# Kernel tuning notes

Hardware: AMD Instinct MI355X
Metric: run time of the kernel (lower is better)

The kernel has to match this reference:

```python
import jax, jax.numpy as jnp
import numpy as np

NUM_Y_STEPS = 10
NUM_TYPES = 3
ANCHOR_DIM = 3 * NUM_Y_STEPS + 1  # 31
EPS = 1e-9


def setup_inputs() -> dict:
    key = jax.random.key(0)
    k1, k2, k3, k4, k5, k6 = jax.random.split(key, 6)
    B, A = 8192, 26
    D = NUM_TYPES * ANCHOR_DIM  # 93
    pred = jax.random.uniform(k1, (B, A, D), dtype=jnp.float32)
    gt = jax.random.uniform(k2, (B, A, D), dtype=jnp.float32)
    pred_hcam = jax.random.uniform(k3, (B,), dtype=jnp.float32) + 1.0
    gt_hcam = jax.random.uniform(k4, (B,), dtype=jnp.float32) + 1.0
    pred_pitch = jax.random.normal(k5, (B,), dtype=jnp.float32)
    gt_pitch = jax.random.normal(k6, (B,), dtype=jnp.float32)
    return {
        'pred_3D_lanes': pred,
        'gt_3D_lanes': gt,
        'pred_hcam': pred_hcam,
        'gt_hcam': gt_hcam,
        'pred_pitch': pred_pitch,
        'gt_pitch': gt_pitch,
    }


def reference(pred_3D_lanes, gt_3D_lanes, pred_hcam, gt_hcam, pred_pitch, gt_pitch):
    B, A, _ = pred_3D_lanes.shape
    K = NUM_Y_STEPS
    pred = pred_3D_lanes.reshape(B, A, NUM_TYPES, ANCHOR_DIM)
    gt = gt_3D_lanes.reshape(B, A, NUM_TYPES, ANCHOR_DIM)

    pred_class = pred[..., -1:]                # [B,A,T,1]
    pred_anchors = pred[..., : 2 * K]          # [B,A,T,2K]
    pred_vis = pred[..., 2 * K : 3 * K]        # [B,A,T,K]
    gt_class = gt[..., -1:]
    gt_anchors = gt[..., : 2 * K]
    gt_vis = gt[..., 2 * K : 3 * K]

    # loss0: binary cross entropy on visibility (note: (1-gt+eps) as in original)
    loss0 = -jnp.sum(
        gt_vis * jnp.log(pred_vis + EPS)
        + (1.0 - gt_vis + EPS) * jnp.log(1.0 - pred_vis + EPS)
    ) / K

    # loss1: binary cross entropy on lane class probability
    loss1 = -jnp.sum(
        gt_class * jnp.log(pred_class + EPS)
        + (1.0 - gt_class) * jnp.log(1.0 - pred_class + EPS)
    )

    # loss2: visibility/class-masked L1 on X-offset and Z anchors
    vis2 = jnp.concatenate([gt_vis, gt_vis], axis=3)  # [B,A,T,2K]
    loss2 = jnp.sum(jnp.abs(gt_class * vis2 * (pred_anchors - gt_anchors)))

    total = loss0 + loss1 + loss2
    return (total, loss0, loss1, loss2)
```

## Files before the change

kernel.cpp:

```cpp
#include <hip/hip_runtime.h>

#define EPSL 1e-9f
#define NGROUPS 638976
#define GPB 128
#define GPW 64
#define WTILE (GPW * 31)
#define NBLOCKS (NGROUPS / GPB)
#define NSLOTS 64

__device__ __forceinline__ void cp_async16(const float* gsrc, float* ldst) {
    __builtin_amdgcn_global_load_lds(
        (const __attribute__((address_space(1))) void*)(uintptr_t)gsrc,
        (__attribute__((address_space(3))) void*)(uint32_t)(uintptr_t)ldst,
        16, 0, 0);
}

__global__ __launch_bounds__(128) void laneline_reduce_kernel(
    const float* __restrict__ pred,
    const float* __restrict__ gt,
    float* __restrict__ ws)
{
    __shared__ float sp[2][WTILE];
    __shared__ float sg[2][WTILE];
    __shared__ float red[6];

    const int lane = threadIdx.x & 63;
    const int wid  = threadIdx.x >> 6;

    const size_t waveFloatBase = ((size_t)blockIdx.x * GPB + wid * GPW) * 31;
    const float* gp = pred + waveFloatBase + lane * 4;
    const float* gg = gt   + waveFloatBase + lane * 4;
#pragma unroll
    for (int r = 0; r < 7; ++r) {
        cp_async16(gp + r * 256, &sp[wid][r * 256]);
        cp_async16(gg + r * 256, &sg[wid][r * 256]);
    }
    if (lane < 48) {
        cp_async16(gp + 1792, &sp[wid][1792]);
        cp_async16(gg + 1792, &sg[wid][1792]);
    }
    __syncthreads();

    const float* lp = &sp[wid][lane * 31];
    const float* lg = &sg[wid][lane * 31];

    const float gcls = lg[30];
    float s0 = 0.f, s2 = 0.f;
#pragma unroll
    for (int i = 0; i < 10; ++i) {
        const float gvis = lg[20 + i];
        s2 += gcls * gvis * (fabsf(lp[i]      - lg[i])
                           + fabsf(lp[10 + i] - lg[10 + i]));
        const float pv = lp[20 + i];
        s0 += gvis * __logf(pv + EPSL)
            + (1.0f - gvis + EPSL) * __logf(1.0f - pv + EPSL);
    }
    const float pc = lp[30];
    float s1 = gcls * __logf(pc + EPSL)
             + (1.0f - gcls) * __logf(1.0f - pc + EPSL);

#pragma unroll
    for (int off = 32; off > 0; off >>= 1) {
        s0 += __shfl_down(s0, off, 64);
        s1 += __shfl_down(s1, off, 64);
        s2 += __shfl_down(s2, off, 64);
    }
    if (lane == 0) { red[wid * 3] = s0; red[wid * 3 + 1] = s1; red[wid * 3 + 2] = s2; }
    __syncthreads();

    if (threadIdx.x == 0) {
        float* slot = ws + (blockIdx.x & (NSLOTS - 1)) * 16;
        atomicAdd(&slot[0], red[0] + red[3]);
        atomicAdd(&slot[1], red[1] + red[4]);
        atomicAdd(&slot[2], red[2] + red[5]);
    }
}

__global__ __launch_bounds__(64) void laneline_finalize_kernel(
    const float* __restrict__ ws, float* __restrict__ out)
{
    const int t = threadIdx.x;
    float v0 = ws[t * 16], v1 = ws[t * 16 + 1], v2 = ws[t * 16 + 2];
#pragma unroll
    for (int off = 32; off > 0; off >>= 1) {
        v0 += __shfl_down(v0, off, 64);
        v1 += __shfl_down(v1, off, 64);
        v2 += __shfl_down(v2, off, 64);
    }
    if (t == 0) {
        const float l0 = -v0 * 0.1f;
        const float l1 = -v1;
        const float l2 =  v2;
        out[0] = l0 + l1 + l2;
        out[1] = l0;
        out[2] = l1;
        out[3] = l2;
    }
}

extern "C" void kernel_launch(void* const* d_in, const int* in_sizes, int n_in,
                              void* d_out, int out_size, void* d_ws, size_t ws_size,
                              hipStream_t stream)
{
    const float* pred = (const float*)d_in[0];
    const float* gt   = (const float*)d_in[1];
    float* ws  = (float*)d_ws;
    float* out = (float*)d_out;

    hipMemsetAsync(ws, 0, NSLOTS * 16 * sizeof(float), stream);

    laneline_reduce_kernel<<<NBLOCKS, 128, 0, stream>>>(pred, gt, ws);
    laneline_finalize_kernel<<<1, 64, 0, stream>>>(ws, out);
}
```

Measured before the change: 185.0 us.

## Make single-wave blocks persistent with double-buffered async LDS tile loads

Switches to 64-thread blocks that each process 8 strided tiles, prefetching the next tile into a second LDS buffer via global_load_lds while computing the current one. Partial sums accumulate in registers across tiles, removing the cross-wave LDS reduction and cutting atomics per element. The per-wave vmcnt threshold assumes a fixed load count per lane, which may not hold for lanes issuing fewer loads, and occupancy per CU changes.

```diff
diff --git a/kernel.cpp b/kernel.cpp
--- a/kernel.cpp
+++ b/kernel.cpp
@@ -2,10 +2,11 @@
 
 #define EPSL 1e-9f
 #define NGROUPS 638976
-#define GPB 128
 #define GPW 64
-#define WTILE (GPW * 31)
-#define NBLOCKS (NGROUPS / GPB)
+#define TFLOATS (GPW * 31)
+#define NTILES (NGROUPS / GPW)
+#define NBLOCKS 1248
+#define NT 8
 #define NSLOTS 64
 
 __device__ __forceinline__ void cp_async16(const float* gsrc, float* ldst) {
@@ -15,49 +16,61 @@
         16, 0, 0);
 }
 
-__global__ __launch_bounds__(128) void laneline_reduce_kernel(
+__global__ __launch_bounds__(64) void laneline_reduce_kernel(
     const float* __restrict__ pred,
     const float* __restrict__ gt,
     float* __restrict__ ws)
 {
-    __shared__ float sp[2][WTILE];
-    __shared__ float sg[2][WTILE];
-    __shared__ float red[6];
+    __shared__ float sp[2][TFLOATS];
+    __shared__ float sg[2][TFLOATS];
 
-    const int lane = threadIdx.x & 63;
-    const int wid  = threadIdx.x >> 6;
+    const int lane = threadIdx.x;
 
-    const size_t waveFloatBase = ((size_t)blockIdx.x * GPB + wid * GPW) * 31;
-    const float* gp = pred + waveFloatBase + lane * 4;
-    const float* gg = gt   + waveFloatBase + lane * 4;
+    auto stage = [&](int b, int tile) {
+        const size_t fb = (size_t)tile * TFLOATS;
+        const float* gp = pred + fb + lane * 4;
+        const float* gg = gt   + fb + lane * 4;
 #pragma unroll
-    for (int r = 0; r < 7; ++r) {
-        cp_async16(gp + r * 256, &sp[wid][r * 256]);
-        cp_async16(gg + r * 256, &sg[wid][r * 256]);
+        for (int r = 0; r < 7; ++r) {
+            cp_async16(gp + r * 256, &sp[b][r * 256]);
+            cp_async16(gg + r * 256, &sg[b][r * 256]);
+        }
+        if (lane < 48) {
+            cp_async16(gp + 1792, &sp[b][1792]);
+            cp_async16(gg + 1792, &sg[b][1792]);
+        }
+    };
+
+    float s0 = 0.f, s1 = 0.f, s2 = 0.f;
+
+    stage(0, blockIdx.x);
+#pragma unroll
+    for (int it = 0; it < NT; ++it) {
+        if (it + 1 < NT) {
+            asm volatile("s_waitcnt lgkmcnt(0)" ::: "memory");
+            stage((it + 1) & 1, blockIdx.x + (it + 1) * NBLOCKS);
+            asm volatile("s_waitcnt vmcnt(16)" ::: "memory");
+        } else {
+            asm volatile("s_waitcnt vmcnt(0)" ::: "memory");
+        }
+
+        const float* lp = &sp[it & 1][lane * 31];
+        const float* lg = &sg[it & 1][lane * 31];
+
+        const float gcls = lg[30];
+#pragma unroll
+        for (int i = 0; i < 10; ++i) {
+            const float gvis = lg[20 + i];
+            s2 += gcls * gvis * (fabsf(lp[i]      - lg[i])
+                               + fabsf(lp[10 + i] - lg[10 + i]));
+            const float pv = lp[20 + i];
+            s0 += gvis * __logf(pv + EPSL)
+                + (1.0f - gvis + EPSL) * __logf(1.0f - pv + EPSL);
+        }
+        const float pc = lp[30];
+        s1 += gcls * __logf(pc + EPSL)
+            + (1.0f - gcls) * __logf(1.0f - pc + EPSL);
     }
-    if (lane < 48) {
-        cp_async16(gp + 1792, &sp[wid][1792]);
-        cp_async16(gg + 1792, &sg[wid][1792]);
-    }
-    __syncthreads();
-
-    const float* lp = &sp[wid][lane * 31];
-    const float* lg = &sg[wid][lane * 31];
-
-    const float gcls = lg[30];
-    float s0 = 0.f, s2 = 0.f;
-#pragma unroll
-    for (int i = 0; i < 10; ++i) {
-        const float gvis = lg[20 + i];
-        s2 += gcls * gvis * (fabsf(lp[i]      - lg[i])
-                           + fabsf(lp[10 + i] - lg[10 + i]));
-        const float pv = lp[20 + i];
-        s0 += gvis * __logf(pv + EPSL)
-            + (1.0f - gvis + EPSL) * __logf(1.0f - pv + EPSL);
-    }
-    const float pc = lp[30];
-    float s1 = gcls * __logf(pc + EPSL)
-             + (1.0f - gcls) * __logf(1.0f - pc + EPSL);
 
 #pragma unroll
     for (int off = 32; off > 0; off >>= 1) {
@@ -65,14 +78,11 @@
         s1 += __shfl_down(s1, off, 64);
         s2 += __shfl_down(s2, off, 64);
     }
-    if (lane == 0) { red[wid * 3] = s0; red[wid * 3 + 1] = s1; red[wid * 3 + 2] = s2; }
-    __syncthreads();
-
-    if (threadIdx.x == 0) {
+    if (lane == 0) {
         float* slot = ws + (blockIdx.x & (NSLOTS - 1)) * 16;
-        atomicAdd(&slot[0], red[0] + red[3]);
-        atomicAdd(&slot[1], red[1] + red[4]);
-        atomicAdd(&slot[2], red[2] + red[5]);
+        atomicAdd(&slot[0], s0);
+        atomicAdd(&slot[1], s1);
+        atomicAdd(&slot[2], s2);
     }
 }
 
@@ -109,6 +119,6 @@
 
     hipMemsetAsync(ws, 0, NSLOTS * 16 * sizeof(float), stream);
 
-    laneline_reduce_kernel<<<NBLOCKS, 128, 0, stream>>>(pred, gt, ws);
+    laneline_reduce_kernel<<<NBLOCKS, 64, 0, stream>>>(pred, gt, ws);
     laneline_finalize_kernel<<<1, 64, 0, stream>>>(ws, out);
 }
```

New measurement: 194.3 us. 1.05x slower.
